# Optimization experiments

Hardware: AMD Instinct MI355X
Metric: run time of the kernel (lower is better)

Reference implementation:

```python
import jax, jax.numpy as jnp
import numpy as np

B, N, E, D = 4, 2048, 2048, 2048  # batch, seq, embedding_dim, out_dim


def setup_inputs() -> dict:
    key = jax.random.key(0)
    k1, k2, k3 = jax.random.split(key, 3)
    x = jax.random.normal(k1, (B, N, E), dtype=jnp.float32)
    # qkv_proj: Linear(E, 3*D). Store weight as [E, 3D] for x @ W.
    W = jax.random.normal(k2, (E, 3 * D), dtype=jnp.float32) * (1.0 / np.sqrt(E))
    b = jax.random.normal(k3, (3 * D,), dtype=jnp.float32) * 0.01
    return {"x": x, "W": W, "b": b}


def reference(x, W, b):
    d = W.shape[1] // 3
    n = x.shape[1]
    qkv = x @ W + b                                   # [B, N, 3D]
    q, k, v = jnp.split(qkv, 3, axis=-1)              # each [B, N, D]
    scale = 1.0 / np.sqrt(d).astype(np.float32)
    att = jnp.einsum('bqd,bkd->bqk', q, k) * scale    # [B, N, N]
    causal = jnp.tril(jnp.ones((n, n), dtype=bool))
    att = jnp.where(causal[None, :, :], att, -jnp.inf)
    # softmax_with_denom: stable softmax, also return the denominator
    m = jnp.max(att, axis=-1, keepdims=True)
    e = jnp.exp(att - m)
    denom = jnp.sum(e, axis=-1)                       # [B, N]
    p = e / denom[..., None]
    y = jnp.einsum('bqk,bkd->bqd', p, v)              # [B, N, D]
    return y, denom
```

## Files before the change

kernel.cpp:

```cpp
#include <hip/hip_runtime.h>

typedef unsigned short u16;
typedef unsigned int   u32;

#define SEQ 2048
#define EMB 2048
#define TD  6144

using bf16x8 = __attribute__((ext_vector_type(8))) __bf16;
using f32x4  = __attribute__((ext_vector_type(4))) float;
using u16x8v = __attribute__((ext_vector_type(8))) u16;

typedef __attribute__((address_space(1))) const void* gas_t;
typedef __attribute__((address_space(3))) void*       las_t;
#define GLOAD16(g, l) __builtin_amdgcn_global_load_lds((gas_t)(g), (las_t)(l), 16, 0, 0)

__device__ __forceinline__ u16 f2bf(float f) {
  u32 u = __float_as_uint(f);
  u += 0x7fffu + ((u >> 16) & 1u);
  return (u16)(u >> 16);
}

__global__ __launch_bounds__(256) void cast_x_kern(const float* __restrict__ x,
                                                   u16* __restrict__ xb) {
  size_t i = ((size_t)blockIdx.x * 256 + threadIdx.x) * 4;
  float4 v = *(const float4*)(x + i);
  ushort4 u;
  u.x = f2bf(v.x); u.y = f2bf(v.y); u.z = f2bf(v.z); u.w = f2bf(v.w);
  *(ushort4*)(xb + i) = u;
}

__global__ __launch_bounds__(256) void castT_W_kern(const float* __restrict__ W,
                                                    u16* __restrict__ Wt) {
  __shared__ float t[64][65];
  int c0 = blockIdx.x * 64, r0 = blockIdx.y * 64;
  int tid = threadIdx.x;
#pragma unroll
  for (int i = 0; i < 4; ++i) {
    int flat = i * 1024 + tid * 4;
    int r = flat >> 6, c = flat & 63;
    float4 v = *(const float4*)(W + (size_t)(r0 + r) * TD + c0 + c);
    t[r][c] = v.x; t[r][c + 1] = v.y; t[r][c + 2] = v.z; t[r][c + 3] = v.w;
  }
  __syncthreads();
#pragma unroll
  for (int i = 0; i < 4; ++i) {
    int flat = i * 1024 + tid * 4;
    int wr = flat >> 6, wc = flat & 63;
    ushort4 u;
    u.x = f2bf(t[wc + 0][wr]); u.y = f2bf(t[wc + 1][wr]);
    u.z = f2bf(t[wc + 2][wr]); u.w = f2bf(t[wc + 3][wr]);
    *(ushort4*)(Wt + (size_t)(c0 + wr) * EMB + r0 + wc) = u;
  }
}

template <int MODE>
__global__ __launch_bounds__(512, 2) void gemm256(const u16* __restrict__ Ab,
                                                  const u16* __restrict__ Bb,
                                                  void* __restrict__ Cb,
                                                  void* __restrict__ Cb2,
                                                  const float* __restrict__ bias) {
  __shared__ char lds[2][65536];

  constexpr int lda = (MODE == 0) ? EMB : 4096;
  constexpr int ldb = (MODE == 0) ? EMB : (MODE == 1) ? 4096 : SEQ;
  constexpr int NWG = (MODE == 0) ? 768 : (MODE == 1) ? 144 : 256;
  constexpr int CPX = NWG / 8;

  int bid = blockIdx.x;
  int wg = (bid & 7) * CPX + (bid >> 3);

  const u16 *A, *Bt;
  int row0, col0, nk;
  size_t coff = 0;
  if constexpr (MODE == 0) {
    A = Ab; Bt = Bb;
    row0 = (wg / 24) * 256; col0 = (wg % 24) * 256; nk = EMB / 64;
  } else if constexpr (MODE == 1) {
    int b = wg / 36, tq = wg % 36;
    int qi = (int)((sqrtf(8.f * (float)tq + 1.f) - 1.f) * 0.5f);
    while ((qi + 1) * (qi + 2) / 2 <= tq) ++qi;
    while (qi * (qi + 1) / 2 > tq) --qi;
    int kj = tq - qi * (qi + 1) / 2;
    A = Ab + (size_t)b * SEQ * 4096;
    Bt = A + 2048;
    row0 = qi * 256; col0 = kj * 256; nk = EMB / 64;
    coff = (size_t)b * SEQ * SEQ;
  } else {
    int b = wg >> 6, qi = (wg >> 3) & 7, nj = wg & 7;
    A = Ab + (size_t)b * SEQ * 4096;
    Bt = Bb + (size_t)b * SEQ * SEQ;
    row0 = qi * 256; col0 = nj * 256; nk = (qi + 1) * 4;
    coff = (size_t)b * SEQ * SEQ;
  }

  int tid = threadIdx.x;
  int wave = tid >> 6, lane = tid & 63;
  int wm = wave >> 2, wn = wave & 3;

  int sbase[8];
#pragma unroll
  for (int i = 0; i < 4; ++i) sbase[i] = 32768 + i * 8192 + wave * 1024;
#pragma unroll
  for (int i = 0; i < 4; ++i)
    sbase[4 + i] = i * 4096 + ((wave < 4) ? wave * 1024 : 16384 + (wave - 4) * 1024);

  auto stageb = [&](int bi, int t, int buf) {
    int ob = sbase[bi];
    int obl = ob + lane * 16;
    int row = (obl & 32767) >> 7;
    int cb = obl & 127;
    int c = ((cb ^ ((row & 7) << 4)) >> 1) + t * 64;
    const u16* src = (ob < 32768) ? (A + (size_t)(row0 + row) * lda + c)
                                  : (Bt + (size_t)(col0 + row) * ldb + c);
    GLOAD16(src, (char*)&lds[buf][0] + ob);
  };

  auto ldA = [&](int buf, int rr, int ks) -> bf16x8 {
    int cb = ks * 64 + (lane >> 4) * 16;
    return *(const bf16x8*)&lds[buf][rr * 128 + (cb ^ ((rr & 7) << 4))];
  };
  auto ldB = [&](int buf, int rr, int ks) -> bf16x8 {
    int cb = ks * 64 + (lane >> 4) * 16;
    return *(const bf16x8*)&lds[buf][32768 + rr * 128 + (cb ^ ((rr & 7) << 4))];
  };

  f32x4 acc[8][4];
#pragma unroll
  for (int m = 0; m < 8; ++m)
#pragma unroll
    for (int n = 0; n < 4; ++n) acc[m][n] = (f32x4){0.f, 0.f, 0.f, 0.f};

#pragma unroll
  for (int bi = 0; bi < 8; ++bi) stageb(bi, 0, 0);
#pragma unroll
  for (int bi = 0; bi < 6; ++bi) stageb(bi, 1, 1);
  asm volatile("s_waitcnt vmcnt(6)" ::: "memory");
  __builtin_amdgcn_s_barrier();

  bf16x8 bfg[4][2];
  for (int t = 0; t < nk; ++t) {
    int cur = t & 1, nxt = cur ^ 1;
#pragma unroll
    for (int p = 0; p < 4; ++p) {
      bf16x8 afg[2][2];
      if (p == 0) {
#pragma unroll
        for (int n = 0; n < 4; ++n)
#pragma unroll
          for (int ks = 0; ks < 2; ++ks)
            bfg[n][ks] = ldB(cur, wn * 64 + n * 16 + (lane & 15), ks);
      }
#pragma unroll
      for (int m = 0; m < 2; ++m)
#pragma unroll
        for (int ks = 0; ks < 2; ++ks)
          afg[m][ks] = ldA(cur, wm * 128 + (p * 2 + m) * 16 + (lane & 15), ks);
      if (p == 0) {
        if (t + 1 < nk) { stageb(6, t + 1, nxt); stageb(7, t + 1, nxt); }
        asm volatile("s_waitcnt lgkmcnt(8)" ::: "memory");
      } else if (t + 2 < nk) {
        stageb(2 * (p - 1), t + 2, cur);
        stageb(2 * (p - 1) + 1, t + 2, cur);
      }
      __builtin_amdgcn_s_barrier();
      asm volatile("s_waitcnt lgkmcnt(0)" ::: "memory");
      __builtin_amdgcn_s_setprio(1);
#pragma unroll
      for (int m = 0; m < 2; ++m)
#pragma unroll
        for (int n = 0; n < 4; ++n)
#pragma unroll
          for (int ks = 0; ks < 2; ++ks)
            acc[p * 2 + m][n] = __builtin_amdgcn_mfma_f32_16x16x32_bf16(
                afg[m][ks], bfg[n][ks], acc[p * 2 + m][n], 0, 0, 0);
      __builtin_amdgcn_s_setprio(0);
      if (p == 3) {
        if (t + 2 < nk)       asm volatile("s_waitcnt vmcnt(6)" ::: "memory");
        else if (t + 1 < nk)  asm volatile("s_waitcnt vmcnt(0)" ::: "memory");
      }
      __builtin_amdgcn_s_barrier();
    }
  }

  int ln = lane & 15;
  int l4 = (lane >> 4) << 2;
  int rb = row0 + wm * 128, cb0 = col0 + wn * 64;
  if constexpr (MODE == 0) {
    if (col0 < 4096) {
      u16* C = (u16*)Cb;
#pragma unroll
      for (int n = 0; n < 4; ++n) {
        float bv = bias[cb0 + n * 16 + ln];
#pragma unroll
        for (int m = 0; m < 8; ++m)
#pragma unroll
          for (int r = 0; r < 4; ++r)
            C[(size_t)(rb + m * 16 + l4 + r) * 4096 + cb0 + n * 16 + ln] =
                f2bf(acc[m][n][r] + bv);
      }
    } else {
      u16* vTb = (u16*)Cb2 + (size_t)(row0 >> 11) * SEQ * SEQ;
      int nbase = row0 & 2047;
      u16 (*T)[264] = (u16(*)[264])(&lds[0][0]);
      int half = wn >> 1;
      int dloc0 = (wn & 1) * 64;
#pragma unroll
      for (int hh = 0; hh < 2; ++hh) {
        if (half == hh) {
#pragma unroll
          for (int n = 0; n < 4; ++n) {
            float bv = bias[cb0 + n * 16 + ln];
            int dl = dloc0 + n * 16 + ln;
#pragma unroll
            for (int m = 0; m < 8; ++m) {
              int nn = wm * 128 + m * 16 + l4;
#pragma unroll
              for (int r = 0; r < 4; ++r)
                T[dl][nn + r] = f2bf(acc[m][n][r] + bv);
            }
          }
        }
        __syncthreads();
        int dl = tid >> 5, nn = (tid & 31) * 8;
#pragma unroll
        for (int it = 0; it < 8; ++it) {
          int loc = it * 16 + dl;
          *(u16x8v*)&vTb[(size_t)(col0 - 4096 + hh * 128 + loc) * SEQ + nbase + nn] =
              *(const u16x8v*)&T[loc][nn];
        }
        __syncthreads();
      }
    }
  } else if constexpr (MODE == 1) {
    float* C = (float*)Cb + coff;
    const float scale = 0.022097086912079608f;
#pragma unroll
    for (int m = 0; m < 8; ++m)
#pragma unroll
      for (int n = 0; n < 4; ++n)
#pragma unroll
        for (int r = 0; r < 4; ++r)
          C[(size_t)(rb + m * 16 + l4 + r) * SEQ + cb0 + n * 16 + ln] =
              acc[m][n][r] * scale;
  } else {
    float* C = (float*)Cb + coff;
#pragma unroll
    for (int m = 0; m < 8; ++m)
#pragma unroll
      for (int n = 0; n < 4; ++n)
#pragma unroll
        for (int r = 0; r < 4; ++r)
          C[(size_t)(rb + m * 16 + l4 + r) * SEQ + cb0 + n * 16 + ln] = acc[m][n][r];
  }
}

__global__ __launch_bounds__(256) void softmax_kern(const float* __restrict__ att,
                                                    u16* __restrict__ P,
                                                    float* __restrict__ denom) {
  int row = blockIdx.x;
  int q = row & (SEQ - 1);
  const float* arow = att + (size_t)row * SEQ;
  u16* prow = P + (size_t)row * 4096;
  int jlen = ((q >> 8) + 1) << 8;
  int tid = threadIdx.x;
  int j0 = tid * 4, j1 = tid * 4 + 1024;
  float NI = -__builtin_inff();
  float4 a0 = make_float4(NI, NI, NI, NI), a1 = a0;
  if (j0 < jlen) a0 = *(const float4*)(arow + j0);
  if (j1 < jlen) a1 = *(const float4*)(arow + j1);
  if (j0 + 0 > q) a0.x = NI;
  if (j0 + 1 > q) a0.y = NI;
  if (j0 + 2 > q) a0.z = NI;
  if (j0 + 3 > q) a0.w = NI;
  if (j1 + 0 > q) a1.x = NI;
  if (j1 + 1 > q) a1.y = NI;
  if (j1 + 2 > q) a1.z = NI;
  if (j1 + 3 > q) a1.w = NI;
  float mx = fmaxf(fmaxf(fmaxf(a0.x, a0.y), fmaxf(a0.z, a0.w)),
                   fmaxf(fmaxf(a1.x, a1.y), fmaxf(a1.z, a1.w)));
#pragma unroll
  for (int off = 32; off; off >>= 1) mx = fmaxf(mx, __shfl_xor(mx, off, 64));
  __shared__ float red[8];
  int wv = tid >> 6;
  if ((tid & 63) == 0) red[wv] = mx;
  __syncthreads();
  mx = fmaxf(fmaxf(red[0], red[1]), fmaxf(red[2], red[3]));
  a0.x = expf(a0.x - mx); a0.y = expf(a0.y - mx);
  a0.z = expf(a0.z - mx); a0.w = expf(a0.w - mx);
  a1.x = expf(a1.x - mx); a1.y = expf(a1.y - mx);
  a1.z = expf(a1.z - mx); a1.w = expf(a1.w - mx);
  float s = (a0.x + a0.y + a0.z + a0.w) + (a1.x + a1.y + a1.z + a1.w);
#pragma unroll
  for (int off = 32; off; off >>= 1) s += __shfl_xor(s, off, 64);
  if ((tid & 63) == 0) red[4 + wv] = s;
  __syncthreads();
  s = red[4] + red[5] + red[6] + red[7];
  float inv = 1.0f / s;
  if (j0 < jlen) {
    ushort4 u;
    u.x = f2bf(a0.x * inv); u.y = f2bf(a0.y * inv);
    u.z = f2bf(a0.z * inv); u.w = f2bf(a0.w * inv);
    *(ushort4*)(prow + j0) = u;
  }
  if (j1 < jlen) {
    ushort4 u;
    u.x = f2bf(a1.x * inv); u.y = f2bf(a1.y * inv);
    u.z = f2bf(a1.z * inv); u.w = f2bf(a1.w * inv);
    *(ushort4*)(prow + j1) = u;
  }
  if (tid == 0) denom[row] = s;
}

extern "C" void kernel_launch(void* const* d_in, const int* in_sizes, int n_in,
                              void* d_out, int out_size, void* d_ws, size_t ws_size,
                              hipStream_t stream) {
  const float* x    = (const float*)d_in[0];
  const float* W    = (const float*)d_in[1];
  const float* bias = (const float*)d_in[2];

  if (ws_size < 201326592u) return;

  char* w = (char*)d_ws;
  u16*   qk  = (u16*)w;
  u16*   vT  = (u16*)(w + 67108864);
  u16*   xb  = (u16*)(w + 100663296);
  u16*   Wt  = (u16*)(w + 134217728);
  float* att = (float*)(w + 134217728);
  u16*   P   = (u16*)(w + 134217728);

  float* y     = (float*)d_out;
  float* denom = y + (size_t)4 * SEQ * SEQ;

  cast_x_kern<<<16384, 256, 0, stream>>>(x, xb);
  castT_W_kern<<<dim3(96, 32), 256, 0, stream>>>(W, Wt);
  gemm256<0><<<768, 512, 0, stream>>>(xb, Wt, qk, vT, bias);
  gemm256<1><<<144, 512, 0, stream>>>(qk, nullptr, att, nullptr, nullptr);
  softmax_kern<<<8192, 256, 0, stream>>>(att, P, denom);
  gemm256<2><<<256, 512, 0, stream>>>(P, vT, y, nullptr, nullptr);
}
```

Measured before the change: 341.4 us.

## Switch GEMMs to 32x32x16 MFMA and make QKV GEMM persistent over three column tiles

Replaces the 16x16x32 MFMA tiling with 32x32x16 bf16 MFMA (f32x16 accumulators) in all three GEMM modes, which changes the LDS fragment loads and the epilogue index mapping. The QKV projection now launches 256 workgroups, each walking three 256-column tiles (Q, K, V) over a continuous 96-step K loop. Accumulators are flushed to the qk buffer at each tile boundary. This aims to cut LDS traffic per MFMA and to fill the machine in a single wave. The cost is a serialized per-tile epilogue inside the loop and less parallelism in the QKV GEMM.

```diff
diff --git a/kernel.cpp b/kernel.cpp
--- a/kernel.cpp
+++ b/kernel.cpp
@@ -8,7 +8,7 @@
 #define TD  6144
 
 using bf16x8 = __attribute__((ext_vector_type(8))) __bf16;
-using f32x4  = __attribute__((ext_vector_type(4))) float;
+using f32x16 = __attribute__((ext_vector_type(16))) float;
 using u16x8v = __attribute__((ext_vector_type(8))) u16;
 
 typedef __attribute__((address_space(1))) const void* gas_t;
@@ -64,18 +64,18 @@
 
   constexpr int lda = (MODE == 0) ? EMB : 4096;
   constexpr int ldb = (MODE == 0) ? EMB : (MODE == 1) ? 4096 : SEQ;
-  constexpr int NWG = (MODE == 0) ? 768 : (MODE == 1) ? 144 : 256;
+  constexpr int NWG = (MODE == 0) ? 256 : (MODE == 1) ? 144 : 256;
   constexpr int CPX = NWG / 8;
 
   int bid = blockIdx.x;
   int wg = (bid & 7) * CPX + (bid >> 3);
 
   const u16 *A, *Bt;
-  int row0, col0, nk;
+  int row0, col0 = 0, c0 = 0, total;
   size_t coff = 0;
   if constexpr (MODE == 0) {
     A = Ab; Bt = Bb;
-    row0 = (wg / 24) * 256; col0 = (wg % 24) * 256; nk = EMB / 64;
+    row0 = (wg >> 3) * 256; c0 = wg & 7; total = 96;
   } else if constexpr (MODE == 1) {
     int b = wg / 36, tq = wg % 36;
     int qi = (int)((sqrtf(8.f * (float)tq + 1.f) - 1.f) * 0.5f);
@@ -84,19 +84,20 @@
     int kj = tq - qi * (qi + 1) / 2;
     A = Ab + (size_t)b * SEQ * 4096;
     Bt = A + 2048;
-    row0 = qi * 256; col0 = kj * 256; nk = EMB / 64;
+    row0 = qi * 256; col0 = kj * 256; total = 32;
     coff = (size_t)b * SEQ * SEQ;
   } else {
     int b = wg >> 6, qi = (wg >> 3) & 7, nj = wg & 7;
     A = Ab + (size_t)b * SEQ * 4096;
     Bt = Bb + (size_t)b * SEQ * SEQ;
-    row0 = qi * 256; col0 = nj * 256; nk = (qi + 1) * 4;
+    row0 = qi * 256; col0 = nj * 256; total = (qi + 1) * 4;
     coff = (size_t)b * SEQ * SEQ;
   }
 
   int tid = threadIdx.x;
   int wave = tid >> 6, lane = tid & 63;
   int wm = wave >> 2, wn = wave & 3;
+  int l31 = lane & 31, hi = lane >> 5;
 
   int sbase[8];
 #pragma unroll
@@ -105,31 +106,59 @@
   for (int i = 0; i < 4; ++i)
     sbase[4 + i] = i * 4096 + ((wave < 4) ? wave * 1024 : 16384 + (wave - 4) * 1024);
 
-  auto stageb = [&](int bi, int t, int buf) {
+  auto stageb = [&](int bi, int ktt, int buf) {
     int ob = sbase[bi];
     int obl = ob + lane * 16;
     int row = (obl & 32767) >> 7;
     int cb = obl & 127;
-    int c = ((cb ^ ((row & 7) << 4)) >> 1) + t * 64;
-    const u16* src = (ob < 32768) ? (A + (size_t)(row0 + row) * lda + c)
-                                  : (Bt + (size_t)(col0 + row) * ldb + c);
+    int tin = (MODE == 0) ? (ktt & 31) : ktt;
+    int c = ((cb ^ ((row & 7) << 4)) >> 1) + tin * 64;
+    const u16* src;
+    if (ob < 32768) {
+      src = A + (size_t)(row0 + row) * lda + c;
+    } else {
+      int cB = (MODE == 0) ? (c0 + 8 * (ktt >> 5)) * 256 : col0;
+      src = Bt + (size_t)(cB + row) * ldb + c;
+    }
     GLOAD16(src, (char*)&lds[buf][0] + ob);
   };
 
   auto ldA = [&](int buf, int rr, int ks) -> bf16x8 {
-    int cb = ks * 64 + (lane >> 4) * 16;
+    int cb = ks * 32 + hi * 16;
     return *(const bf16x8*)&lds[buf][rr * 128 + (cb ^ ((rr & 7) << 4))];
   };
   auto ldB = [&](int buf, int rr, int ks) -> bf16x8 {
-    int cb = ks * 64 + (lane >> 4) * 16;
+    int cb = ks * 32 + hi * 16;
     return *(const bf16x8*)&lds[buf][32768 + rr * 128 + (cb ^ ((rr & 7) << 4))];
   };
 
-  f32x4 acc[8][4];
-#pragma unroll
-  for (int m = 0; m < 8; ++m)
-#pragma unroll
-    for (int n = 0; n < 4; ++n) acc[m][n] = (f32x4){0.f, 0.f, 0.f, 0.f};
+  f32x16 acc[4][2];
+#pragma unroll
+  for (int m = 0; m < 4; ++m)
+#pragma unroll
+    for (int n = 0; n < 2; ++n) acc[m][n] = (f32x16)(0.f);
+
+  int rb = row0 + wm * 128, cb0w = wn * 64;
+
+  auto dump_qk = [&](int colbase) {
+    u16* C = (u16*)Cb;
+#pragma unroll
+    for (int n = 0; n < 2; ++n) {
+      int col = colbase + cb0w + n * 32 + l31;
+      float bv = bias[col];
+#pragma unroll
+      for (int m = 0; m < 4; ++m)
+#pragma unroll
+        for (int r = 0; r < 16; ++r) {
+          int row = rb + m * 32 + (r & 3) + 8 * (r >> 2) + 4 * hi;
+          C[(size_t)row * 4096 + col] = f2bf(acc[m][n][r] + bv);
+        }
+    }
+#pragma unroll
+    for (int m = 0; m < 4; ++m)
+#pragma unroll
+      for (int n = 0; n < 2; ++n) acc[m][n] = (f32x16)(0.f);
+  };
 
 #pragma unroll
   for (int bi = 0; bi < 8; ++bi) stageb(bi, 0, 0);
@@ -138,120 +167,140 @@
   asm volatile("s_waitcnt vmcnt(6)" ::: "memory");
   __builtin_amdgcn_s_barrier();
 
-  bf16x8 bfg[4][2];
-  for (int t = 0; t < nk; ++t) {
-    int cur = t & 1, nxt = cur ^ 1;
-#pragma unroll
-    for (int p = 0; p < 4; ++p) {
-      bf16x8 afg[2][2];
-      if (p == 0) {
-#pragma unroll
-        for (int n = 0; n < 4; ++n)
-#pragma unroll
-          for (int ks = 0; ks < 2; ++ks)
-            bfg[n][ks] = ldB(cur, wn * 64 + n * 16 + (lane & 15), ks);
+  bf16x8 bfg[2][4];
+  for (int kt = 0; kt < total; ++kt) {
+    int cur = kt & 1, nxt = cur ^ 1;
+    bool pf1 = (kt + 1 < total), pf2 = (kt + 2 < total);
+    bf16x8 afg[4];
+
+#pragma unroll
+    for (int n = 0; n < 2; ++n)
+#pragma unroll
+      for (int ks = 0; ks < 4; ++ks)
+        bfg[n][ks] = ldB(cur, wn * 64 + n * 32 + l31, ks);
+#pragma unroll
+    for (int ks = 0; ks < 4; ++ks)
+      afg[ks] = ldA(cur, wm * 128 + l31, ks);
+    if (pf1) { stageb(6, kt + 1, nxt); stageb(7, kt + 1, nxt); }
+    __builtin_amdgcn_s_setprio(1);
+#pragma unroll
+    for (int n = 0; n < 2; ++n)
+#pragma unroll
+      for (int ks = 0; ks < 4; ++ks)
+        acc[0][n] = __builtin_amdgcn_mfma_f32_32x32x16_bf16(
+            afg[ks], bfg[n][ks], acc[0][n], 0, 0, 0);
+    __builtin_amdgcn_s_setprio(0);
+    __builtin_amdgcn_s_barrier();
+
+#pragma unroll
+    for (int ks = 0; ks < 4; ++ks)
+      afg[ks] = ldA(cur, wm * 128 + 32 + l31, ks);
+    if (pf2) { stageb(0, kt + 2, cur); stageb(1, kt + 2, cur); }
+    __builtin_amdgcn_s_setprio(1);
+#pragma unroll
+    for (int n = 0; n < 2; ++n)
+#pragma unroll
+      for (int ks = 0; ks < 4; ++ks)
+        acc[1][n] = __builtin_amdgcn_mfma_f32_32x32x16_bf16(
+            afg[ks], bfg[n][ks], acc[1][n], 0, 0, 0);
+    __builtin_amdgcn_s_setprio(0);
+
+#pragma unroll
+    for (int ks = 0; ks < 4; ++ks)
+      afg[ks] = ldA(cur, wm * 128 + 64 + l31, ks);
+    if (pf2) { stageb(2, kt + 2, cur); stageb(3, kt + 2, cur); }
+    __builtin_amdgcn_s_setprio(1);
+#pragma unroll
+    for (int n = 0; n < 2; ++n)
+#pragma unroll
+      for (int ks = 0; ks < 4; ++ks)
+        acc[2][n] = __builtin_amdgcn_mfma_f32_32x32x16_bf16(
+            afg[ks], bfg[n][ks], acc[2][n], 0, 0, 0);
+    __builtin_amdgcn_s_setprio(0);
+    __builtin_amdgcn_s_barrier();
+
+#pragma unroll
+    for (int ks = 0; ks < 4; ++ks)
+      afg[ks] = ldA(cur, wm * 128 + 96 + l31, ks);
+    if (pf2) { stageb(4, kt + 2, cur); stageb(5, kt + 2, cur); }
+    __builtin_amdgcn_s_setprio(1);
+#pragma unroll
+    for (int n = 0; n < 2; ++n)
+#pragma unroll
+      for (int ks = 0; ks < 4; ++ks)
+        acc[3][n] = __builtin_amdgcn_mfma_f32_32x32x16_bf16(
+            afg[ks], bfg[n][ks], acc[3][n], 0, 0, 0);
+    __builtin_amdgcn_s_setprio(0);
+    if (pf2)      asm volatile("s_waitcnt vmcnt(6)" ::: "memory");
+    else if (pf1) asm volatile("s_waitcnt vmcnt(0)" ::: "memory");
+    __builtin_amdgcn_s_barrier();
+
+    if constexpr (MODE == 0) {
+      if ((kt & 31) == 31 && kt != total - 1)
+        dump_qk((c0 + 8 * (kt >> 5)) * 256);
+    }
+  }
+
+  if constexpr (MODE == 0) {
+    int col0v = (c0 + 16) * 256;
+    u16* vTb = (u16*)Cb2 + (size_t)(row0 >> 11) * SEQ * SEQ;
+    int nbase = row0 & 2047;
+    u16 (*T)[264] = (u16(*)[264])(&lds[0][0]);
+    int half = wn >> 1;
+    int dloc0 = (wn & 1) * 64;
+#pragma unroll
+    for (int hh = 0; hh < 2; ++hh) {
+      if (half == hh) {
+#pragma unroll
+        for (int n = 0; n < 2; ++n) {
+          int col = col0v + cb0w + n * 32 + l31;
+          float bv = bias[col];
+          int dl = dloc0 + n * 32 + l31;
+#pragma unroll
+          for (int m = 0; m < 4; ++m)
+#pragma unroll
+            for (int r = 0; r < 16; ++r)
+              T[dl][wm * 128 + m * 32 + (r & 3) + 8 * (r >> 2) + 4 * hi] =
+                  f2bf(acc[m][n][r] + bv);
+        }
       }
-#pragma unroll
-      for (int m = 0; m < 2; ++m)
-#pragma unroll
-        for (int ks = 0; ks < 2; ++ks)
-          afg[m][ks] = ldA(cur, wm * 128 + (p * 2 + m) * 16 + (lane & 15), ks);
-      if (p == 0) {
-        if (t + 1 < nk) { stageb(6, t + 1, nxt); stageb(7, t + 1, nxt); }
-        asm volatile("s_waitcnt lgkmcnt(8)" ::: "memory");
-      } else if (t + 2 < nk) {
-        stageb(2 * (p - 1), t + 2, cur);
-        stageb(2 * (p - 1) + 1, t + 2, cur);
+      __syncthreads();
+      int dl = tid >> 5, nn = (tid & 31) * 8;
+#pragma unroll
+      for (int it = 0; it < 8; ++it) {
+        int loc = it * 16 + dl;
+        *(u16x8v*)&vTb[(size_t)(col0v - 4096 + hh * 128 + loc) * SEQ + nbase + nn] =
+            *(const u16x8v*)&T[loc][nn];
       }
-      __builtin_amdgcn_s_barrier();
-      asm volatile("s_waitcnt lgkmcnt(0)" ::: "memory");
-      __builtin_amdgcn_s_setprio(1);
-#pragma unroll
-      for (int m = 0; m < 2; ++m)
-#pragma unroll
-        for (int n = 0; n < 4; ++n)
-#pragma unroll
-          for (int ks = 0; ks < 2; ++ks)
-            acc[p * 2 + m][n] = __builtin_amdgcn_mfma_f32_16x16x32_bf16(
-                afg[m][ks], bfg[n][ks], acc[p * 2 + m][n], 0, 0, 0);
-      __builtin_amdgcn_s_setprio(0);
-      if (p == 3) {
-        if (t + 2 < nk)       asm volatile("s_waitcnt vmcnt(6)" ::: "memory");
-        else if (t + 1 < nk)  asm volatile("s_waitcnt vmcnt(0)" ::: "memory");
-      }
-      __builtin_amdgcn_s_barrier();
-    }
-  }
-
-  int ln = lane & 15;
-  int l4 = (lane >> 4) << 2;
-  int rb = row0 + wm * 128, cb0 = col0 + wn * 64;
-  if constexpr (MODE == 0) {
-    if (col0 < 4096) {
-      u16* C = (u16*)Cb;
-#pragma unroll
-      for (int n = 0; n < 4; ++n) {
-        float bv = bias[cb0 + n * 16 + ln];
-#pragma unroll
-        for (int m = 0; m < 8; ++m)
-#pragma unroll
-          for (int r = 0; r < 4; ++r)
-            C[(size_t)(rb + m * 16 + l4 + r) * 4096 + cb0 + n * 16 + ln] =
-                f2bf(acc[m][n][r] + bv);
-      }
-    } else {
-      u16* vTb = (u16*)Cb2 + (size_t)(row0 >> 11) * SEQ * SEQ;
-      int nbase = row0 & 2047;
-      u16 (*T)[264] = (u16(*)[264])(&lds[0][0]);
-      int half = wn >> 1;
-      int dloc0 = (wn & 1) * 64;
-#pragma unroll
-      for (int hh = 0; hh < 2; ++hh) {
-        if (half == hh) {
-#pragma unroll
-          for (int n = 0; n < 4; ++n) {
-            float bv = bias[cb0 + n * 16 + ln];
-            int dl = dloc0 + n * 16 + ln;
-#pragma unroll
-            for (int m = 0; m < 8; ++m) {
-              int nn = wm * 128 + m * 16 + l4;
-#pragma unroll
-              for (int r = 0; r < 4; ++r)
-                T[dl][nn + r] = f2bf(acc[m][n][r] + bv);
-            }
-          }
-        }
-        __syncthreads();
-        int dl = tid >> 5, nn = (tid & 31) * 8;
-#pragma unroll
-        for (int it = 0; it < 8; ++it) {
-          int loc = it * 16 + dl;
-          *(u16x8v*)&vTb[(size_t)(col0 - 4096 + hh * 128 + loc) * SEQ + nbase + nn] =
-              *(const u16x8v*)&T[loc][nn];
-        }
-        __syncthreads();
-      }
+      __syncthreads();
     }
   } else if constexpr (MODE == 1) {
     float* C = (float*)Cb + coff;
     const float scale = 0.022097086912079608f;
 #pragma unroll
-    for (int m = 0; m < 8; ++m)
-#pragma unroll
-      for (int n = 0; n < 4; ++n)
-#pragma unroll
-        for (int r = 0; r < 4; ++r)
-          C[(size_t)(rb + m * 16 + l4 + r) * SEQ + cb0 + n * 16 + ln] =
-              acc[m][n][r] * scale;
+    for (int n = 0; n < 2; ++n) {
+      int col = col0 + cb0w + n * 32 + l31;
+#pragma unroll
+      for (int m = 0; m < 4; ++m)
+#pragma unroll
+        for (int r = 0; r < 16; ++r) {
+          int row = rb + m * 32 + (r & 3) + 8 * (r >> 2) + 4 * hi;
+          C[(size_t)row * SEQ + col] = acc[m][n][r] * scale;
+        }
+    }
   } else {
     float* C = (float*)Cb + coff;
 #pragma unroll
-    for (int m = 0; m < 8; ++m)
-#pragma unroll
-      for (int n = 0; n < 4; ++n)
-#pragma unroll
-        for (int r = 0; r < 4; ++r)
-          C[(size_t)(rb + m * 16 + l4 + r) * SEQ + cb0 + n * 16 + ln] = acc[m][n][r];
+    for (int n = 0; n < 2; ++n) {
+      int col = col0 + cb0w + n * 32 + l31;
+#pragma unroll
+      for (int m = 0; m < 4; ++m)
+#pragma unroll
+        for (int r = 0; r < 16; ++r) {
+          int row = rb + m * 32 + (r & 3) + 8 * (r >> 2) + 4 * hi;
+          C[(size_t)row * SEQ + col] = acc[m][n][r];
+        }
+    }
   }
 }
 
@@ -334,7 +383,7 @@
 
   cast_x_kern<<<16384, 256, 0, stream>>>(x, xb);
   castT_W_kern<<<dim3(96, 32), 256, 0, stream>>>(W, Wt);
-  gemm256<0><<<768, 512, 0, stream>>>(xb, Wt, qk, vT, bias);
+  gemm256<0><<<256, 512, 0, stream>>>(xb, Wt, qk, vT, bias);
   gemm256<1><<<144, 512, 0, stream>>>(qk, nullptr, att, nullptr, nullptr);
   softmax_kern<<<8192, 256, 0, stream>>>(att, P, denom);
   gemm256<2><<<256, 512, 0, stream>>>(P, vT, y, nullptr, nullptr);
```

Result: slower. 531.3 us (+55.6%).

## Shrink GEMM tiles to 128x128 with 4 waves, finer causal tiling, fuse cast kernels

Applied to the files above, without the earlier changes.

Replaces the 256x256, 8-wave GEMM with a 128x128, 4-wave variant and re-derives the pipelined prefetch schedule, work-group mapping and epilogues for the smaller tile. The finer tiles reduce wasted causal work in the QK^T and PV GEMMs, since softmax now only reads 128-aligned prefixes, and they launch many more workgroups for better CU occupancy and load balance. PV workgroups are ordered longest-first. The x cast and W transpose-cast are merged into one launch. The cost is lower data reuse per tile (more global/LDS traffic per FLOP) in the large projection GEMM.

```diff
diff --git a/kernel.cpp b/kernel.cpp
--- a/kernel.cpp
+++ b/kernel.cpp
@@ -21,237 +21,227 @@
   return (u16)(u >> 16);
 }
 
-__global__ __launch_bounds__(256) void cast_x_kern(const float* __restrict__ x,
-                                                   u16* __restrict__ xb) {
-  size_t i = ((size_t)blockIdx.x * 256 + threadIdx.x) * 4;
-  float4 v = *(const float4*)(x + i);
-  ushort4 u;
-  u.x = f2bf(v.x); u.y = f2bf(v.y); u.z = f2bf(v.z); u.w = f2bf(v.w);
-  *(ushort4*)(xb + i) = u;
-}
-
-__global__ __launch_bounds__(256) void castT_W_kern(const float* __restrict__ W,
-                                                    u16* __restrict__ Wt) {
-  __shared__ float t[64][65];
-  int c0 = blockIdx.x * 64, r0 = blockIdx.y * 64;
+__global__ __launch_bounds__(256) void prep_kern(const float* __restrict__ x,
+                                                 u16* __restrict__ xb,
+                                                 const float* __restrict__ W,
+                                                 u16* __restrict__ Wt) {
+  int bid = blockIdx.x;
   int tid = threadIdx.x;
-#pragma unroll
-  for (int i = 0; i < 4; ++i) {
-    int flat = i * 1024 + tid * 4;
-    int r = flat >> 6, c = flat & 63;
-    float4 v = *(const float4*)(W + (size_t)(r0 + r) * TD + c0 + c);
-    t[r][c] = v.x; t[r][c + 1] = v.y; t[r][c + 2] = v.z; t[r][c + 3] = v.w;
-  }
-  __syncthreads();
-#pragma unroll
-  for (int i = 0; i < 4; ++i) {
-    int flat = i * 1024 + tid * 4;
-    int wr = flat >> 6, wc = flat & 63;
+  if (bid < 16384) {
+    size_t i = ((size_t)bid * 256 + tid) * 4;
+    float4 v = *(const float4*)(x + i);
     ushort4 u;
-    u.x = f2bf(t[wc + 0][wr]); u.y = f2bf(t[wc + 1][wr]);
-    u.z = f2bf(t[wc + 2][wr]); u.w = f2bf(t[wc + 3][wr]);
-    *(ushort4*)(Wt + (size_t)(c0 + wr) * EMB + r0 + wc) = u;
+    u.x = f2bf(v.x); u.y = f2bf(v.y); u.z = f2bf(v.z); u.w = f2bf(v.w);
+    *(ushort4*)(xb + i) = u;
+  } else {
+    __shared__ float t[64][65];
+    int wb = bid - 16384;
+    int c0 = (wb % 96) * 64, r0 = (wb / 96) * 64;
+#pragma unroll
+    for (int i = 0; i < 4; ++i) {
+      int flat = i * 1024 + tid * 4;
+      int r = flat >> 6, c = flat & 63;
+      float4 v = *(const float4*)(W + (size_t)(r0 + r) * TD + c0 + c);
+      t[r][c] = v.x; t[r][c + 1] = v.y; t[r][c + 2] = v.z; t[r][c + 3] = v.w;
+    }
+    __syncthreads();
+#pragma unroll
+    for (int i = 0; i < 4; ++i) {
+      int flat = i * 1024 + tid * 4;
+      int wr = flat >> 6, wc = flat & 63;
+      ushort4 u;
+      u.x = f2bf(t[wc + 0][wr]); u.y = f2bf(t[wc + 1][wr]);
+      u.z = f2bf(t[wc + 2][wr]); u.w = f2bf(t[wc + 3][wr]);
+      *(ushort4*)(Wt + (size_t)(c0 + wr) * EMB + r0 + wc) = u;
+    }
   }
 }
 
 template <int MODE>
-__global__ __launch_bounds__(512, 2) void gemm256(const u16* __restrict__ Ab,
+__global__ __launch_bounds__(256, 2) void gemm128(const u16* __restrict__ Ab,
                                                   const u16* __restrict__ Bb,
                                                   void* __restrict__ Cb,
-                                                  void* __restrict__ Cb2,
+                                                  u16* __restrict__ Cb2,
                                                   const float* __restrict__ bias) {
-  __shared__ char lds[2][65536];
-
+  __shared__ char lds[2][32768];
   constexpr int lda = (MODE == 0) ? EMB : 4096;
   constexpr int ldb = (MODE == 0) ? EMB : (MODE == 1) ? 4096 : SEQ;
-  constexpr int NWG = (MODE == 0) ? 768 : (MODE == 1) ? 144 : 256;
-  constexpr int CPX = NWG / 8;
 
   int bid = blockIdx.x;
-  int wg = (bid & 7) * CPX + (bid >> 3);
-
   const u16 *A, *Bt;
   int row0, col0, nk;
   size_t coff = 0;
   if constexpr (MODE == 0) {
+    int wg = (bid & 7) * 384 + (bid >> 3);
     A = Ab; Bt = Bb;
-    row0 = (wg / 24) * 256; col0 = (wg % 24) * 256; nk = EMB / 64;
+    row0 = (wg / 48) * 128; col0 = (wg % 48) * 128; nk = EMB / 64;
   } else if constexpr (MODE == 1) {
-    int b = wg / 36, tq = wg % 36;
+    constexpr int CPX = 544 / 8;
+    int wg = (bid & 7) * CPX + (bid >> 3);
+    int b = wg / 136, tq = wg % 136;
     int qi = (int)((sqrtf(8.f * (float)tq + 1.f) - 1.f) * 0.5f);
     while ((qi + 1) * (qi + 2) / 2 <= tq) ++qi;
     while (qi * (qi + 1) / 2 > tq) --qi;
     int kj = tq - qi * (qi + 1) / 2;
     A = Ab + (size_t)b * SEQ * 4096;
     Bt = A + 2048;
-    row0 = qi * 256; col0 = kj * 256; nk = EMB / 64;
+    row0 = qi * 128; col0 = kj * 128; nk = EMB / 64;
     coff = (size_t)b * SEQ * SEQ;
   } else {
-    int b = wg >> 6, qi = (wg >> 3) & 7, nj = wg & 7;
+    int xcd = bid & 7, idx = bid >> 3;
+    int qi = 15 - (idx >> 3);
+    int g = xcd * 8 + (idx & 7);
+    int b = g >> 4, nj = g & 15;
     A = Ab + (size_t)b * SEQ * 4096;
     Bt = Bb + (size_t)b * SEQ * SEQ;
-    row0 = qi * 256; col0 = nj * 256; nk = (qi + 1) * 4;
+    row0 = qi * 128; col0 = nj * 128; nk = (qi + 1) * 2;
     coff = (size_t)b * SEQ * SEQ;
   }
 
   int tid = threadIdx.x;
   int wave = tid >> 6, lane = tid & 63;
-  int wm = wave >> 2, wn = wave & 3;
+  int wm = wave >> 1, wn = wave & 1;
+  int ln = lane & 15;
 
   int sbase[8];
 #pragma unroll
-  for (int i = 0; i < 4; ++i) sbase[i] = 32768 + i * 8192 + wave * 1024;
-#pragma unroll
-  for (int i = 0; i < 4; ++i)
-    sbase[4 + i] = i * 4096 + ((wave < 4) ? wave * 1024 : 16384 + (wave - 4) * 1024);
+  for (int i = 0; i < 4; ++i) sbase[i] = 16384 + i * 4096 + wave * 1024;
+#pragma unroll
+  for (int i = 0; i < 4; ++i) sbase[4 + i] = i * 4096 + wave * 1024;
 
   auto stageb = [&](int bi, int t, int buf) {
     int ob = sbase[bi];
     int obl = ob + lane * 16;
-    int row = (obl & 32767) >> 7;
+    int row = (obl & 16383) >> 7;
     int cb = obl & 127;
     int c = ((cb ^ ((row & 7) << 4)) >> 1) + t * 64;
-    const u16* src = (ob < 32768) ? (A + (size_t)(row0 + row) * lda + c)
+    const u16* src = (ob < 16384) ? (A + (size_t)(row0 + row) * lda + c)
                                   : (Bt + (size_t)(col0 + row) * ldb + c);
     GLOAD16(src, (char*)&lds[buf][0] + ob);
   };
-
   auto ldA = [&](int buf, int rr, int ks) -> bf16x8 {
     int cb = ks * 64 + (lane >> 4) * 16;
     return *(const bf16x8*)&lds[buf][rr * 128 + (cb ^ ((rr & 7) << 4))];
   };
   auto ldB = [&](int buf, int rr, int ks) -> bf16x8 {
     int cb = ks * 64 + (lane >> 4) * 16;
-    return *(const bf16x8*)&lds[buf][32768 + rr * 128 + (cb ^ ((rr & 7) << 4))];
+    return *(const bf16x8*)&lds[buf][16384 + rr * 128 + (cb ^ ((rr & 7) << 4))];
   };
 
-  f32x4 acc[8][4];
-#pragma unroll
-  for (int m = 0; m < 8; ++m)
+  f32x4 acc[4][4];
+#pragma unroll
+  for (int m = 0; m < 4; ++m)
 #pragma unroll
     for (int n = 0; n < 4; ++n) acc[m][n] = (f32x4){0.f, 0.f, 0.f, 0.f};
 
 #pragma unroll
   for (int bi = 0; bi < 8; ++bi) stageb(bi, 0, 0);
-#pragma unroll
-  for (int bi = 0; bi < 6; ++bi) stageb(bi, 1, 1);
+  stageb(0, 1, 1); stageb(1, 1, 1); stageb(2, 1, 1); stageb(3, 1, 1);
+  stageb(4, 1, 1); stageb(6, 1, 1);
   asm volatile("s_waitcnt vmcnt(6)" ::: "memory");
   __builtin_amdgcn_s_barrier();
 
   bf16x8 bfg[4][2];
   for (int t = 0; t < nk; ++t) {
     int cur = t & 1, nxt = cur ^ 1;
-#pragma unroll
-    for (int p = 0; p < 4; ++p) {
-      bf16x8 afg[2][2];
-      if (p == 0) {
-#pragma unroll
-        for (int n = 0; n < 4; ++n)
-#pragma unroll
-          for (int ks = 0; ks < 2; ++ks)
-            bfg[n][ks] = ldB(cur, wn * 64 + n * 16 + (lane & 15), ks);
-      }
-#pragma unroll
-      for (int m = 0; m < 2; ++m)
+    bool pf1 = (t + 1 < nk), pf2 = (t + 2 < nk);
+    bf16x8 afg[2][2];
+#pragma unroll
+    for (int n = 0; n < 4; ++n)
+#pragma unroll
+      for (int ks = 0; ks < 2; ++ks)
+        bfg[n][ks] = ldB(cur, wn * 64 + n * 16 + ln, ks);
+#pragma unroll
+    for (int m = 0; m < 2; ++m)
+#pragma unroll
+      for (int ks = 0; ks < 2; ++ks)
+        afg[m][ks] = ldA(cur, wm * 64 + m * 16 + ln, ks);
+    if (pf1) { stageb(5, t + 1, nxt); stageb(7, t + 1, nxt); }
+    __builtin_amdgcn_s_setprio(1);
+#pragma unroll
+    for (int m = 0; m < 2; ++m)
+#pragma unroll
+      for (int n = 0; n < 4; ++n)
 #pragma unroll
         for (int ks = 0; ks < 2; ++ks)
-          afg[m][ks] = ldA(cur, wm * 128 + (p * 2 + m) * 16 + (lane & 15), ks);
-      if (p == 0) {
-        if (t + 1 < nk) { stageb(6, t + 1, nxt); stageb(7, t + 1, nxt); }
-        asm volatile("s_waitcnt lgkmcnt(8)" ::: "memory");
-      } else if (t + 2 < nk) {
-        stageb(2 * (p - 1), t + 2, cur);
-        stageb(2 * (p - 1) + 1, t + 2, cur);
-      }
-      __builtin_amdgcn_s_barrier();
-      asm volatile("s_waitcnt lgkmcnt(0)" ::: "memory");
-      __builtin_amdgcn_s_setprio(1);
-#pragma unroll
-      for (int m = 0; m < 2; ++m)
-#pragma unroll
-        for (int n = 0; n < 4; ++n)
-#pragma unroll
-          for (int ks = 0; ks < 2; ++ks)
-            acc[p * 2 + m][n] = __builtin_amdgcn_mfma_f32_16x16x32_bf16(
-                afg[m][ks], bfg[n][ks], acc[p * 2 + m][n], 0, 0, 0);
-      __builtin_amdgcn_s_setprio(0);
-      if (p == 3) {
-        if (t + 2 < nk)       asm volatile("s_waitcnt vmcnt(6)" ::: "memory");
-        else if (t + 1 < nk)  asm volatile("s_waitcnt vmcnt(0)" ::: "memory");
-      }
-      __builtin_amdgcn_s_barrier();
+          acc[m][n] = __builtin_amdgcn_mfma_f32_16x16x32_bf16(
+              afg[m][ks], bfg[n][ks], acc[m][n], 0, 0, 0);
+    __builtin_amdgcn_s_setprio(0);
+    __builtin_amdgcn_s_barrier();
+#pragma unroll
+    for (int m = 0; m < 2; ++m)
+#pragma unroll
+      for (int ks = 0; ks < 2; ++ks)
+        afg[m][ks] = ldA(cur, wm * 64 + (2 + m) * 16 + ln, ks);
+    if (pf2) {
+      stageb(0, t + 2, cur); stageb(1, t + 2, cur); stageb(2, t + 2, cur);
+      stageb(3, t + 2, cur); stageb(4, t + 2, cur); stageb(6, t + 2, cur);
     }
-  }
-
-  int ln = lane & 15;
+    __builtin_amdgcn_s_setprio(1);
+#pragma unroll
+    for (int m = 0; m < 2; ++m)
+#pragma unroll
+      for (int n = 0; n < 4; ++n)
+#pragma unroll
+        for (int ks = 0; ks < 2; ++ks)
+          acc[2 + m][n] = __builtin_amdgcn_mfma_f32_16x16x32_bf16(
+              afg[m][ks], bfg[n][ks], acc[2 + m][n], 0, 0, 0);
+    __builtin_amdgcn_s_setprio(0);
+    if (pf2)      asm volatile("s_waitcnt vmcnt(6)" ::: "memory");
+    else if (pf1) asm volatile("s_waitcnt vmcnt(0)" ::: "memory");
+    __builtin_amdgcn_s_barrier();
+  }
+
   int l4 = (lane >> 4) << 2;
-  int rb = row0 + wm * 128, cb0 = col0 + wn * 64;
   if constexpr (MODE == 0) {
     if (col0 < 4096) {
       u16* C = (u16*)Cb;
+      int rb = row0 + wm * 64, cb0 = col0 + wn * 64;
 #pragma unroll
       for (int n = 0; n < 4; ++n) {
         float bv = bias[cb0 + n * 16 + ln];
 #pragma unroll
-        for (int m = 0; m < 8; ++m)
+        for (int m = 0; m < 4; ++m)
 #pragma unroll
           for (int r = 0; r < 4; ++r)
             C[(size_t)(rb + m * 16 + l4 + r) * 4096 + cb0 + n * 16 + ln] =
                 f2bf(acc[m][n][r] + bv);
       }
     } else {
-      u16* vTb = (u16*)Cb2 + (size_t)(row0 >> 11) * SEQ * SEQ;
+      u16* vTb = Cb2 + (size_t)(row0 >> 11) * SEQ * SEQ;
       int nbase = row0 & 2047;
-      u16 (*T)[264] = (u16(*)[264])(&lds[0][0]);
-      int half = wn >> 1;
-      int dloc0 = (wn & 1) * 64;
-#pragma unroll
-      for (int hh = 0; hh < 2; ++hh) {
-        if (half == hh) {
-#pragma unroll
-          for (int n = 0; n < 4; ++n) {
-            float bv = bias[cb0 + n * 16 + ln];
-            int dl = dloc0 + n * 16 + ln;
-#pragma unroll
-            for (int m = 0; m < 8; ++m) {
-              int nn = wm * 128 + m * 16 + l4;
-#pragma unroll
-              for (int r = 0; r < 4; ++r)
-                T[dl][nn + r] = f2bf(acc[m][n][r] + bv);
-            }
-          }
-        }
-        __syncthreads();
-        int dl = tid >> 5, nn = (tid & 31) * 8;
-#pragma unroll
-        for (int it = 0; it < 8; ++it) {
-          int loc = it * 16 + dl;
-          *(u16x8v*)&vTb[(size_t)(col0 - 4096 + hh * 128 + loc) * SEQ + nbase + nn] =
-              *(const u16x8v*)&T[loc][nn];
-        }
-        __syncthreads();
+      u16 (*T)[136] = (u16(*)[136])(&lds[0][0]);
+#pragma unroll
+      for (int n = 0; n < 4; ++n) {
+        int dl = wn * 64 + n * 16 + ln;
+        float bv = bias[col0 + dl];
+#pragma unroll
+        for (int m = 0; m < 4; ++m)
+#pragma unroll
+          for (int r = 0; r < 4; ++r)
+            T[dl][wm * 64 + m * 16 + l4 + r] = f2bf(acc[m][n][r] + bv);
+      }
+      __syncthreads();
+      int nn = (tid & 15) * 8;
+#pragma unroll
+      for (int it = 0; it < 8; ++it) {
+        int loc = it * 16 + (tid >> 4);
+        *(u16x8v*)&vTb[(size_t)(col0 - 4096 + loc) * SEQ + nbase + nn] =
+            *(const u16x8v*)&T[loc][nn];
       }
     }
-  } else if constexpr (MODE == 1) {
+  } else {
     float* C = (float*)Cb + coff;
-    const float scale = 0.022097086912079608f;
-#pragma unroll
-    for (int m = 0; m < 8; ++m)
+    int rb = row0 + wm * 64, cb0 = col0 + wn * 64;
+    const float scale = (MODE == 1) ? 0.022097086912079608f : 1.0f;
+#pragma unroll
+    for (int m = 0; m < 4; ++m)
 #pragma unroll
       for (int n = 0; n < 4; ++n)
 #pragma unroll
         for (int r = 0; r < 4; ++r)
           C[(size_t)(rb + m * 16 + l4 + r) * SEQ + cb0 + n * 16 + ln] =
               acc[m][n][r] * scale;
-  } else {
-    float* C = (float*)Cb + coff;
-#pragma unroll
-    for (int m = 0; m < 8; ++m)
-#pragma unroll
-      for (int n = 0; n < 4; ++n)
-#pragma unroll
-        for (int r = 0; r < 4; ++r)
-          C[(size_t)(rb + m * 16 + l4 + r) * SEQ + cb0 + n * 16 + ln] = acc[m][n][r];
   }
 }
 
@@ -262,7 +252,7 @@
   int q = row & (SEQ - 1);
   const float* arow = att + (size_t)row * SEQ;
   u16* prow = P + (size_t)row * 4096;
-  int jlen = ((q >> 8) + 1) << 8;
+  int jlen = ((q >> 7) + 1) << 7;
   int tid = threadIdx.x;
   int j0 = tid * 4, j1 = tid * 4 + 1024;
   float NI = -__builtin_inff();
@@ -332,10 +322,9 @@
   float* y     = (float*)d_out;
   float* denom = y + (size_t)4 * SEQ * SEQ;
 
-  cast_x_kern<<<16384, 256, 0, stream>>>(x, xb);
-  castT_W_kern<<<dim3(96, 32), 256, 0, stream>>>(W, Wt);
-  gemm256<0><<<768, 512, 0, stream>>>(xb, Wt, qk, vT, bias);
-  gemm256<1><<<144, 512, 0, stream>>>(qk, nullptr, att, nullptr, nullptr);
+  prep_kern<<<19456, 256, 0, stream>>>(x, xb, W, Wt);
+  gemm128<0><<<3072, 256, 0, stream>>>(xb, Wt, qk, vT, bias);
+  gemm128<1><<<544, 256, 0, stream>>>(qk, nullptr, att, nullptr, nullptr);
   softmax_kern<<<8192, 256, 0, stream>>>(att, P, denom);
-  gemm256<2><<<256, 512, 0, stream>>>(P, vT, y, nullptr, nullptr);
-}
+  gemm128<2><<<1024, 256, 0, stream>>>(P, vT, y, nullptr, nullptr);
+}
```

Measured after the change: 382.2 us. 1.12x slower.
